# Optimization experiments

Measured on AMD Instinct MI355X. Metric: run time of the kernel, lower is better.

## Reference

```python
import jax, jax.numpy as jnp
import numpy as np

ROUTING_ITER = 3
EPS = 1e-7  # keras backend epsilon


def squash(x, axis=-1):
    # squash_factor * unit_vector, computed in one pass
    sq = jnp.sum(jnp.square(x), axis=axis, keepdims=True)
    return (sq / (1.0 + sq)) * x / jnp.sqrt(sq + EPS)


def setup_inputs() -> dict:
    key = jax.random.key(0)
    k1, k2 = jax.random.split(key)
    B, P, pD = 64, 2048, 16
    N, D = 32, 32
    x = jax.random.normal(k1, (B, P, pD), dtype=jnp.float32)
    # transform weights, stddev 0.1 as in build()
    w = 0.1 * jax.random.normal(k2, (P, N, D, pD), dtype=jnp.float32)
    return {"x": x, "w": w}


def reference(x, w):
    # x: (B, P, pD); w: (P, N, D, pD)
    # prediction u_hat: (B, P, N, D)  == matmul(w, x[...,None]) in original
    pred = jnp.einsum('pndq,bpq->bpnd', w, x)
    B, P, N, D = pred.shape
    b = jnp.zeros((B, P, N, 1), dtype=pred.dtype)  # routing logits

    def weighted_squash(b_logits):
        c = jax.nn.softmax(b_logits, axis=2)              # (B,P,N,1)
        s = jnp.sum(c * pred, axis=1, keepdims=True)      # (B,1,N,D)
        return squash(s, axis=-1)                         # (B,1,N,D)

    for _ in range(ROUTING_ITER):
        v = weighted_squash(b)
        # agreement: <u_hat, v> over D, broadcast over P
        agreement = jnp.sum(pred * v, axis=-1, keepdims=True)  # (B,P,N,1)
        b = b + agreement

    v = weighted_squash(b)                                # (B,1,N,D)
    return v.reshape(B, N, D)
```

## Files before the change

### kernel.cpp

```cpp
#include <hip/hip_runtime.h>
#include <math.h>

#define B_SZ 64
#define P_SZ 2048
#define PD   16
#define N_SZ 32
#define D_SZ 32
#define ND   1024
#define PC   8
#define BC   8
#define NPC  (P_SZ / PC)
#define NBC  (B_SZ / BC)
#define PP   16
#define NPCH (P_SZ / PP)

typedef _Float16 half2_t __attribute__((ext_vector_type(2)));

__device__ __forceinline__ float dot2acc(unsigned a, unsigned b, float acc) {
#if __has_builtin(__builtin_amdgcn_fdot2)
    return __builtin_amdgcn_fdot2(__builtin_bit_cast(half2_t, a),
                                  __builtin_bit_cast(half2_t, b), acc, false);
#else
    const half2_t ha = __builtin_bit_cast(half2_t, a);
    const half2_t hb = __builtin_bit_cast(half2_t, b);
    return acc + (float)ha[0] * (float)hb[0] + (float)ha[1] * (float)hb[1];
#endif
}

__device__ __forceinline__ unsigned packh2(float a, float b) {
    half2_t h; h[0] = (_Float16)a; h[1] = (_Float16)b;
    return __builtin_bit_cast(unsigned, h);
}

__device__ __forceinline__ float4 unpackh4(uint2 u) {
    const half2_t lo = __builtin_bit_cast(half2_t, u.x);
    const half2_t hi = __builtin_bit_cast(half2_t, u.y);
    return make_float4((float)lo[0], (float)lo[1], (float)hi[0], (float)hi[1]);
}

__device__ __forceinline__ float dot4(const float4 a, const float4 b) {
    return a.x * b.x + a.y * b.y + a.z * b.z + a.w * b.w;
}

__global__ __launch_bounds__(256) void repack_w(const float4* __restrict__ w4,
                                                uint4* __restrict__ w2u4) {
    const size_t g = (size_t)blockIdx.x * 256 + threadIdx.x;
    const int p    = (int)(g >> 10);
    const int q    = (int)((g >> 8) & 3);
    const int t    = (int)(g & 255);
    const size_t f0 = ((size_t)p * 1024 + 4 * t + q) * 4;
    const float4 a = w4[f0], b = w4[f0 + 1], c = w4[f0 + 2], d = w4[f0 + 3];
    uint4 o0, o1;
    o0.x = packh2(a.x, a.y); o0.y = packh2(a.z, a.w);
    o0.z = packh2(b.x, b.y); o0.w = packh2(b.z, b.w);
    o1.x = packh2(c.x, c.y); o1.y = packh2(c.z, c.w);
    o1.z = packh2(d.x, d.y); o1.w = packh2(d.z, d.w);
    w2u4[((size_t)p * 8 + 2 * q) * 256 + t]     = o0;
    w2u4[((size_t)p * 8 + 2 * q + 1) * 256 + t] = o1;
}

__global__ __launch_bounds__(256) void repack_x(const float4* __restrict__ x4,
                                                uint4* __restrict__ x2) {
    const size_t g = (size_t)blockIdx.x * 256 + threadIdx.x;
    const float4 a = x4[g * 2], b = x4[g * 2 + 1];
    uint4 o;
    o.x = packh2(a.x, a.y); o.y = packh2(a.z, a.w);
    o.z = packh2(b.x, b.y); o.w = packh2(b.z, b.w);
    x2[g] = o;
}

__device__ __forceinline__ float4 predict(const uint4 (&W)[8], const unsigned* X) {
    float s; float4 pr;
    s = dot2acc(W[0].x, X[0], 0.f); s = dot2acc(W[0].y, X[1], s);
    s = dot2acc(W[0].z, X[2], s);   s = dot2acc(W[0].w, X[3], s);
    s = dot2acc(W[1].x, X[4], s);   s = dot2acc(W[1].y, X[5], s);
    s = dot2acc(W[1].z, X[6], s);   s = dot2acc(W[1].w, X[7], s);
    pr.x = s;
    s = dot2acc(W[2].x, X[0], 0.f); s = dot2acc(W[2].y, X[1], s);
    s = dot2acc(W[2].z, X[2], s);   s = dot2acc(W[2].w, X[3], s);
    s = dot2acc(W[3].x, X[4], s);   s = dot2acc(W[3].y, X[5], s);
    s = dot2acc(W[3].z, X[6], s);   s = dot2acc(W[3].w, X[7], s);
    pr.y = s;
    s = dot2acc(W[4].x, X[0], 0.f); s = dot2acc(W[4].y, X[1], s);
    s = dot2acc(W[4].z, X[2], s);   s = dot2acc(W[4].w, X[3], s);
    s = dot2acc(W[5].x, X[4], s);   s = dot2acc(W[5].y, X[5], s);
    s = dot2acc(W[5].z, X[6], s);   s = dot2acc(W[5].w, X[7], s);
    pr.z = s;
    s = dot2acc(W[6].x, X[0], 0.f); s = dot2acc(W[6].y, X[1], s);
    s = dot2acc(W[6].z, X[2], s);   s = dot2acc(W[6].w, X[3], s);
    s = dot2acc(W[7].x, X[4], s);   s = dot2acc(W[7].y, X[5], s);
    s = dot2acc(W[7].z, X[6], s);   s = dot2acc(W[7].w, X[7], s);
    pr.w = s;
    return pr;
}

template <int MODE, bool STORE_PRED>
__global__ __launch_bounds__(256, 4) void fused_pass(
    const uint4* __restrict__ x2, const uint4* __restrict__ w2,
    const float* __restrict__ v_in, float* __restrict__ b_io,
    uint2* __restrict__ s_part, uint2* __restrict__ pred_out)
{
    const int t     = threadIdx.x;
    const int gblk  = blockIdx.x;
    const int xcd   = gblk & 7;
    const int j     = gblk >> 3;
    const int pc    = xcd * (NPC / 8) + (j >> 3);
    const int bc    = j & 7;
    const int p0    = pc * PC, b0 = bc * BC;
    const int n     = t >> 3;
    const int wv    = t >> 6;
    const int lane  = t & 63;

    __shared__ uint2 vs2[BC * 256];
    __shared__ float sden[2][16];

    if (MODE != 0) {
        const float4* vg = (const float4*)v_in;
        #pragma unroll
        for (int i = 0; i < BC; ++i) {
            const int idx = t + 256 * i;
            const float4 vv = vg[(size_t)(b0 + (idx >> 8)) * 256 + (idx & 255)];
            uint2 u = { packh2(vv.x, vv.y), packh2(vv.z, vv.w) };
            vs2[idx] = u;
        }
        __syncthreads();
    }

    float4 sacc[BC];
    #pragma unroll
    for (int i = 0; i < BC; ++i) sacc[i] = make_float4(0.f, 0.f, 0.f, 0.f);

    const uint4* wbase = w2 + (size_t)p0 * (8 * 256) + t;
    const uint4* xbase = x2 + (size_t)b0 * P_SZ * 2;

    for (int pl = 0; pl < PC; ++pl) {
        const int p = p0 + pl;
        uint4 W[8];
        #pragma unroll
        for (int k = 0; k < 8; ++k) W[k] = wbase[(size_t)pl * 2048 + k * 256];

        if (MODE == 0) {
            #pragma unroll
            for (int j2 = 0; j2 < BC; ++j2) {
                const uint4* xp = xbase + ((size_t)j2 * P_SZ + p) * 2;
                const uint4 xa = xp[0], xb = xp[1];
                const unsigned X[8] = {xa.x, xa.y, xa.z, xa.w, xb.x, xb.y, xb.z, xb.w};
                const float4 pr = predict(W, X);
                if (STORE_PRED) {
                    uint2 u = { packh2(pr.x, pr.y), packh2(pr.z, pr.w) };
                    pred_out[((size_t)(b0 + j2) * P_SZ + p) * 256 + t] = u;
                }
                sacc[j2].x += pr.x * (1.0f / 32.0f);
                sacc[j2].y += pr.y * (1.0f / 32.0f);
                sacc[j2].z += pr.z * (1.0f / 32.0f);
                sacc[j2].w += pr.w * (1.0f / 32.0f);
            }
        } else {
            #pragma unroll
            for (int h = 0; h < 2; ++h) {
                const int par = h;
                float4 pr[4];
                float  ap[4], ee[4], bold[4];
                if (MODE == 2) {
                    #pragma unroll
                    for (int j2 = 0; j2 < 4; ++j2)
                        bold[j2] = b_io[((size_t)(b0 + h * 4 + j2) * P_SZ + p) * N_SZ + n];
                }
                #pragma unroll
                for (int j2 = 0; j2 < 4; ++j2) {
                    const int bl = h * 4 + j2;
                    const uint4* xp = xbase + ((size_t)bl * P_SZ + p) * 2;
                    const uint4 xa = xp[0], xb = xp[1];
                    const unsigned X[8] = {xa.x, xa.y, xa.z, xa.w, xb.x, xb.y, xb.z, xb.w};
                    pr[j2] = predict(W, X);
                    ap[j2] = dot4(pr[j2], unpackh4(vs2[bl * 256 + t]));
                }
                #pragma unroll
                for (int j2 = 0; j2 < 4; ++j2) {
                    ap[j2] += __shfl_xor(ap[j2], 1);
                    ap[j2] += __shfl_xor(ap[j2], 2);
                    ap[j2] += __shfl_xor(ap[j2], 4);
                }
                #pragma unroll
                for (int j2 = 0; j2 < 4; ++j2) {
                    const size_t bidx = ((size_t)(b0 + h * 4 + j2) * P_SZ + p) * N_SZ + n;
                    const float bnew = (MODE == 1) ? ap[j2] : (bold[j2] + ap[j2]);
                    if ((t & 7) == 0) b_io[bidx] = bnew;
                    ee[j2] = __expf(bnew);
                }
                #pragma unroll
                for (int j2 = 0; j2 < 4; ++j2) {
                    float ps = ee[j2];
                    ps += __shfl_xor(ps, 8);
                    ps += __shfl_xor(ps, 16);
                    ps += __shfl_xor(ps, 32);
                    ap[j2] = ps;
                }
                if (lane == 0) {
                    #pragma unroll
                    for (int j2 = 0; j2 < 4; ++j2) sden[par][j2 * 4 + wv] = ap[j2];
                }
                __syncthreads();
                #pragma unroll
                for (int j2 = 0; j2 < 4; ++j2) {
                    const int bl = h * 4 + j2;
                    const float4 dd = *(const float4*)&sden[par][j2 * 4];
                    const float c = ee[j2] * __builtin_amdgcn_rcpf(dd.x + dd.y + dd.z + dd.w);
                    sacc[bl].x += c * pr[j2].x; sacc[bl].y += c * pr[j2].y;
                    sacc[bl].z += c * pr[j2].z; sacc[bl].w += c * pr[j2].w;
                }
            }
        }
    }

    #pragma unroll
    for (int j2 = 0; j2 < BC; ++j2) {
        uint2 u = { packh2(sacc[j2].x, sacc[j2].y), packh2(sacc[j2].z, sacc[j2].w) };
        s_part[((size_t)pc * B_SZ + (b0 + j2)) * 256 + t] = u;
    }
}

__global__ __launch_bounds__(256, 4) void routing_wave(
    const uint4* __restrict__ pred, const float* __restrict__ vsum,
    uint4* __restrict__ s_part)
{
    const int t    = threadIdx.x;
    const int wv   = t >> 6;
    const int lane = t & 63;
    const int g    = blockIdx.x * 4 + wv;
    const int b    = g >> 7;
    const int pch  = g & (NPCH - 1);
    const int p0   = pch * PP;

    unsigned vlo[4], vhi[4];
    {
        const float4* vp = (const float4*)vsum + ((size_t)b * 256 + 2 * lane);
        const float4 a0 = vp[0],   a1 = vp[1];
        const float4 b0 = vp[128], b1 = vp[129];
        vlo[0] = packh2(a0.x, a0.y); vlo[1] = packh2(a0.z, a0.w);
        vlo[2] = packh2(a1.x, a1.y); vlo[3] = packh2(a1.z, a1.w);
        vhi[0] = packh2(b0.x, b0.y); vhi[1] = packh2(b0.z, b0.w);
        vhi[2] = packh2(b1.x, b1.y); vhi[3] = packh2(b1.z, b1.w);
    }

    float slo[8], shi[8];
    #pragma unroll
    for (int i = 0; i < 8; ++i) { slo[i] = 0.f; shi[i] = 0.f; }

    const uint4* pb = pred + ((size_t)b * P_SZ + p0) * 128 + lane;

    #pragma unroll 4
    for (int pl = 0; pl < PP; ++pl) {
        const uint4 A  = pb[0];
        const uint4 Bq = pb[64];
        pb += 128;
        float alo = 0.f, ahi = 0.f;
        alo = dot2acc(A.x,  vlo[0], alo); alo = dot2acc(A.y,  vlo[1], alo);
        alo = dot2acc(A.z,  vlo[2], alo); alo = dot2acc(A.w,  vlo[3], alo);
        ahi = dot2acc(Bq.x, vhi[0], ahi); ahi = dot2acc(Bq.y, vhi[1], ahi);
        ahi = dot2acc(Bq.z, vhi[2], ahi); ahi = dot2acc(Bq.w, vhi[3], ahi);
        alo += __shfl_xor(alo, 1);  alo += __shfl_xor(alo, 2);
        ahi += __shfl_xor(ahi, 1);  ahi += __shfl_xor(ahi, 2);
        const float elo = __expf(alo), ehi = __expf(ahi);
        float den = elo + ehi;
        den += __shfl_xor(den, 4);   den += __shfl_xor(den, 8);
        den += __shfl_xor(den, 16);  den += __shfl_xor(den, 32);
        const float r   = __builtin_amdgcn_rcpf(den);
        const float clo = elo * r, chi = ehi * r;
        const unsigned XA[4] = {A.x,  A.y,  A.z,  A.w};
        const unsigned XB[4] = {Bq.x, Bq.y, Bq.z, Bq.w};
        #pragma unroll
        for (int i = 0; i < 4; ++i) {
            const half2_t ha = __builtin_bit_cast(half2_t, XA[i]);
            const half2_t hb = __builtin_bit_cast(half2_t, XB[i]);
            slo[2 * i]     += clo * (float)ha[0];
            slo[2 * i + 1] += clo * (float)ha[1];
            shi[2 * i]     += chi * (float)hb[0];
            shi[2 * i + 1] += chi * (float)hb[1];
        }
    }

    uint4 o0, o1;
    o0.x = packh2(slo[0], slo[1]); o0.y = packh2(slo[2], slo[3]);
    o0.z = packh2(slo[4], slo[5]); o0.w = packh2(slo[6], slo[7]);
    o1.x = packh2(shi[0], shi[1]); o1.y = packh2(shi[2], shi[3]);
    o1.z = packh2(shi[4], shi[5]); o1.w = packh2(shi[6], shi[7]);
    uint4* sp = s_part + ((size_t)pch * B_SZ + b) * 128;
    sp[lane]      = o0;
    sp[64 + lane] = o1;
}

template <int VMODE>
__global__ __launch_bounds__(256) void reduce_squash2(
    const uint2* __restrict__ s_part, float* __restrict__ dst)
{
    const int t   = threadIdx.x;
    const int b   = blockIdx.x;
    const int q   = blockIdx.y;
    const int l   = t & 63;
    const int sub = t >> 6;
    const int nd4 = q * 64 + l;

    float4 s = make_float4(0.f, 0.f, 0.f, 0.f);
    for (int i = 0; i < NPCH / 4; ++i) {
        const int pcid = sub + 4 * i;
        const float4 v = unpackh4(s_part[((size_t)pcid * B_SZ + b) * 256 + nd4]);
        s.x += v.x; s.y += v.y; s.z += v.z; s.w += v.w;
    }
    __shared__ float4 red[3][64];
    if (sub > 0) red[sub - 1][l] = s;
    __syncthreads();
    if (t < 64) {
        #pragma unroll
        for (int wvi = 0; wvi < 3; ++wvi) {
            const float4 r = red[wvi][t];
            s.x += r.x; s.y += r.y; s.z += r.z; s.w += r.w;
        }
        float sq = dot4(s, s);
        sq += __shfl_xor(sq, 1);
        sq += __shfl_xor(sq, 2);
        sq += __shfl_xor(sq, 4);
        const float f = sq / ((1.0f + sq) * sqrtf(sq + 1e-7f));
        float4 o = make_float4(f * s.x, f * s.y, f * s.z, f * s.w);
        if (VMODE == 1) {
            const float4 old = ((const float4*)dst)[(size_t)b * 256 + nd4];
            o.x += old.x; o.y += old.y; o.z += old.z; o.w += old.w;
        }
        ((float4*)dst)[(size_t)b * 256 + nd4] = o;
    }
}

__global__ __launch_bounds__(256) void reduce_squash(
    const uint2* __restrict__ s_part, float* __restrict__ dst)
{
    const int t  = threadIdx.x;
    const int b  = blockIdx.x;
    const int q  = blockIdx.y;
    const int l  = t & 63;
    const int sub = t >> 6;
    const int nd4 = q * 64 + l;

    float4 s = make_float4(0.f, 0.f, 0.f, 0.f);
    for (int i = 0; i < NPC / 4; ++i) {
        const int pcid = sub + 4 * i;
        const float4 v = unpackh4(s_part[((size_t)pcid * B_SZ + b) * 256 + nd4]);
        s.x += v.x; s.y += v.y; s.z += v.z; s.w += v.w;
    }
    __shared__ float4 red[3][64];
    if (sub > 0) red[sub - 1][l] = s;
    __syncthreads();
    if (t < 64) {
        #pragma unroll
        for (int wvi = 0; wvi < 3; ++wvi) {
            const float4 r = red[wvi][t];
            s.x += r.x; s.y += r.y; s.z += r.z; s.w += r.w;
        }
        float sq = dot4(s, s);
        sq += __shfl_xor(sq, 1);
        sq += __shfl_xor(sq, 2);
        sq += __shfl_xor(sq, 4);
        const float f = sq / ((1.0f + sq) * sqrtf(sq + 1e-7f));
        ((float4*)dst)[(size_t)b * 256 + nd4] =
            make_float4(f * s.x, f * s.y, f * s.z, f * s.w);
    }
}

extern "C" void kernel_launch(void* const* d_in, const int* in_sizes, int n_in,
                              void* d_out, int out_size, void* d_ws, size_t ws_size,
                              hipStream_t stream)
{
    const float* x = (const float*)d_in[0];
    const float* w = (const float*)d_in[1];
    float* out = (float*)d_out;
    float* ws  = (float*)d_ws;

    float*    v_buf  = ws;
    uint2*    s_part = (uint2*)(ws + 65536);
    unsigned* w2     = (unsigned*)(ws + 8454144);
    uint4*    x2     = (uint4*)(ws + 25231360);
    uint2*    pred   = (uint2*)(ws + 26279936);
    float*    b_fb   = ws + 26279936;
    const size_t need = 93388800ull * 4ull;

    repack_w<<<dim3(8192),  dim3(256), 0, stream>>>((const float4*)w, (uint4*)w2);
    repack_x<<<dim3(1024),  dim3(256), 0, stream>>>((const float4*)x, (uint4*)x2);

    dim3 fg(NPC * NBC), fb(256);
    dim3 rg(B_SZ, 4), rb(256);

    if (ws_size >= need) {
        fused_pass<0, true><<<fg, fb, 0, stream>>>(x2, (const uint4*)w2, nullptr,
                                                   nullptr, s_part, pred);
        reduce_squash<<<rg, rb, 0, stream>>>(s_part, v_buf);

        routing_wave<<<dim3(2048), dim3(256), 0, stream>>>(
            (const uint4*)pred, v_buf, (uint4*)s_part);
        reduce_squash2<1><<<rg, rb, 0, stream>>>(s_part, v_buf);

        routing_wave<<<dim3(2048), dim3(256), 0, stream>>>(
            (const uint4*)pred, v_buf, (uint4*)s_part);
        reduce_squash2<1><<<rg, rb, 0, stream>>>(s_part, v_buf);

        routing_wave<<<dim3(2048), dim3(256), 0, stream>>>(
            (const uint4*)pred, v_buf, (uint4*)s_part);
        reduce_squash2<2><<<rg, rb, 0, stream>>>(s_part, out);
    } else {
        fused_pass<0, false><<<fg, fb, 0, stream>>>(x2, (const uint4*)w2, nullptr,
                                                    nullptr, s_part, nullptr);
        reduce_squash<<<rg, rb, 0, stream>>>(s_part, v_buf);
        fused_pass<1, false><<<fg, fb, 0, stream>>>(x2, (const uint4*)w2, v_buf,
                                                    b_fb, s_part, nullptr);
        reduce_squash<<<rg, rb, 0, stream>>>(s_part, v_buf);
        fused_pass<2, false><<<fg, fb, 0, stream>>>(x2, (const uint4*)w2, v_buf,
                                                    b_fb, s_part, nullptr);
        reduce_squash<<<rg, rb, 0, stream>>>(s_part, v_buf);
        fused_pass<2, false><<<fg, fb, 0, stream>>>(x2, (const uint4*)w2, v_buf,
                                                    b_fb, s_part, nullptr);
        reduce_squash<<<rg, rb, 0, stream>>>(s_part, out);
    }
}
```

Baseline: 464.4 us.

## Merge repack kernels, add nontemporal pred traffic, XCD remap and prefetch routing loads

Merges the two repack kernels into one launch to save a kernel launch. Pred stores in the fused pass and pred loads in routing_wave become nontemporal, keeping the large pred stream from evicting other cache lines. routing_wave gets an XCD-aware block-to-batch mapping, a higher occupancy hint, and a fully unrolled loop that prefetches the next pred row. The risks are register pressure from the occupancy bound together with the prefetch, and changed L2 locality.

```diff
diff --git a/kernel.cpp b/kernel.cpp
--- a/kernel.cpp
+++ b/kernel.cpp
@@ -15,6 +15,8 @@
 #define NPCH (P_SZ / PP)
 
 typedef _Float16 half2_t __attribute__((ext_vector_type(2)));
+typedef unsigned u32x4 __attribute__((ext_vector_type(4)));
+typedef unsigned u32x2 __attribute__((ext_vector_type(2)));
 
 __device__ __forceinline__ float dot2acc(unsigned a, unsigned b, float acc) {
 #if __has_builtin(__builtin_amdgcn_fdot2)
@@ -42,31 +44,43 @@
     return a.x * b.x + a.y * b.y + a.z * b.z + a.w * b.w;
 }
 
-__global__ __launch_bounds__(256) void repack_w(const float4* __restrict__ w4,
-                                                uint4* __restrict__ w2u4) {
-    const size_t g = (size_t)blockIdx.x * 256 + threadIdx.x;
-    const int p    = (int)(g >> 10);
-    const int q    = (int)((g >> 8) & 3);
-    const int t    = (int)(g & 255);
-    const size_t f0 = ((size_t)p * 1024 + 4 * t + q) * 4;
-    const float4 a = w4[f0], b = w4[f0 + 1], c = w4[f0 + 2], d = w4[f0 + 3];
-    uint4 o0, o1;
-    o0.x = packh2(a.x, a.y); o0.y = packh2(a.z, a.w);
-    o0.z = packh2(b.x, b.y); o0.w = packh2(b.z, b.w);
-    o1.x = packh2(c.x, c.y); o1.y = packh2(c.z, c.w);
-    o1.z = packh2(d.x, d.y); o1.w = packh2(d.z, d.w);
-    w2u4[((size_t)p * 8 + 2 * q) * 256 + t]     = o0;
-    w2u4[((size_t)p * 8 + 2 * q + 1) * 256 + t] = o1;
-}
-
-__global__ __launch_bounds__(256) void repack_x(const float4* __restrict__ x4,
-                                                uint4* __restrict__ x2) {
-    const size_t g = (size_t)blockIdx.x * 256 + threadIdx.x;
-    const float4 a = x4[g * 2], b = x4[g * 2 + 1];
-    uint4 o;
-    o.x = packh2(a.x, a.y); o.y = packh2(a.z, a.w);
-    o.z = packh2(b.x, b.y); o.w = packh2(b.z, b.w);
-    x2[g] = o;
+__device__ __forceinline__ uint4 ntload4(const uint4* p) {
+    const u32x4 v = __builtin_nontemporal_load((const u32x4*)p);
+    uint4 r; r.x = v[0]; r.y = v[1]; r.z = v[2]; r.w = v[3];
+    return r;
+}
+__device__ __forceinline__ void ntstore2(uint2* p, uint2 x) {
+    u32x2 v; v[0] = x.x; v[1] = x.y;
+    __builtin_nontemporal_store(v, (u32x2*)p);
+}
+
+__global__ __launch_bounds__(256) void repack_wx(
+    const float4* __restrict__ w4, uint4* __restrict__ w2u4,
+    const float4* __restrict__ x4, uint4* __restrict__ x2)
+{
+    const int blk = blockIdx.x;
+    if (blk < 8192) {
+        const size_t g = (size_t)blk * 256 + threadIdx.x;
+        const int p    = (int)(g >> 10);
+        const int q    = (int)((g >> 8) & 3);
+        const int t    = (int)(g & 255);
+        const size_t f0 = ((size_t)p * 1024 + 4 * t + q) * 4;
+        const float4 a = w4[f0], b = w4[f0 + 1], c = w4[f0 + 2], d = w4[f0 + 3];
+        uint4 o0, o1;
+        o0.x = packh2(a.x, a.y); o0.y = packh2(a.z, a.w);
+        o0.z = packh2(b.x, b.y); o0.w = packh2(b.z, b.w);
+        o1.x = packh2(c.x, c.y); o1.y = packh2(c.z, c.w);
+        o1.z = packh2(d.x, d.y); o1.w = packh2(d.z, d.w);
+        w2u4[((size_t)p * 8 + 2 * q) * 256 + t]     = o0;
+        w2u4[((size_t)p * 8 + 2 * q + 1) * 256 + t] = o1;
+    } else {
+        const size_t g = (size_t)(blk - 8192) * 256 + threadIdx.x;
+        const float4 a = x4[g * 2], b = x4[g * 2 + 1];
+        uint4 o;
+        o.x = packh2(a.x, a.y); o.y = packh2(a.z, a.w);
+        o.z = packh2(b.x, b.y); o.w = packh2(b.z, b.w);
+        x2[g] = o;
+    }
 }
 
 __device__ __forceinline__ float4 predict(const uint4 (&W)[8], const unsigned* X) {
@@ -148,7 +162,7 @@
                 const float4 pr = predict(W, X);
                 if (STORE_PRED) {
                     uint2 u = { packh2(pr.x, pr.y), packh2(pr.z, pr.w) };
-                    pred_out[((size_t)(b0 + j2) * P_SZ + p) * 256 + t] = u;
+                    ntstore2(&pred_out[((size_t)(b0 + j2) * P_SZ + p) * 256 + t], u);
                 }
                 sacc[j2].x += pr.x * (1.0f / 32.0f);
                 sacc[j2].y += pr.y * (1.0f / 32.0f);
@@ -220,16 +234,18 @@
     }
 }
 
-__global__ __launch_bounds__(256, 4) void routing_wave(
+__global__ __launch_bounds__(256, 8) void routing_wave(
     const uint4* __restrict__ pred, const float* __restrict__ vsum,
     uint4* __restrict__ s_part)
 {
     const int t    = threadIdx.x;
     const int wv   = t >> 6;
     const int lane = t & 63;
-    const int g    = blockIdx.x * 4 + wv;
-    const int b    = g >> 7;
-    const int pch  = g & (NPCH - 1);
+    const int xcd  = blockIdx.x & 7;
+    const int jj   = blockIdx.x >> 3;
+    const int gl   = jj * 4 + wv;
+    const int b    = xcd * 8 + (gl >> 7);
+    const int pch  = gl & (NPCH - 1);
     const int p0   = pch * PP;
 
     unsigned vlo[4], vhi[4];
@@ -249,11 +265,16 @@
 
     const uint4* pb = pred + ((size_t)b * P_SZ + p0) * 128 + lane;
 
-    #pragma unroll 4
+    uint4 A  = ntload4(pb);
+    uint4 Bq = ntload4(pb + 64);
+
+    #pragma unroll
     for (int pl = 0; pl < PP; ++pl) {
-        const uint4 A  = pb[0];
-        const uint4 Bq = pb[64];
-        pb += 128;
+        uint4 An, Bn;
+        if (pl + 1 < PP) {
+            An = ntload4(pb + 128);
+            Bn = ntload4(pb + 192);
+        }
         float alo = 0.f, ahi = 0.f;
         alo = dot2acc(A.x,  vlo[0], alo); alo = dot2acc(A.y,  vlo[1], alo);
         alo = dot2acc(A.z,  vlo[2], alo); alo = dot2acc(A.w,  vlo[3], alo);
@@ -278,6 +299,8 @@
             shi[2 * i]     += chi * (float)hb[0];
             shi[2 * i + 1] += chi * (float)hb[1];
         }
+        A = An; Bq = Bn;
+        pb += 128;
     }
 
     uint4 o0, o1;
@@ -382,8 +405,8 @@
     float*    b_fb   = ws + 26279936;
     const size_t need = 93388800ull * 4ull;
 
-    repack_w<<<dim3(8192),  dim3(256), 0, stream>>>((const float4*)w, (uint4*)w2);
-    repack_x<<<dim3(1024),  dim3(256), 0, stream>>>((const float4*)x, (uint4*)x2);
+    repack_wx<<<dim3(9216), dim3(256), 0, stream>>>((const float4*)w, (uint4*)w2,
+                                                    (const float4*)x, (uint4*)x2);
 
     dim3 fg(NPC * NBC), fb(256);
     dim3 rg(B_SZ, 4), rb(256);
```

Result: slower. 570.1 us (+22.8%).
